# Kernel optimization log

Measured on AMD Instinct MI355X. Metric: run time of the kernel, lower is better.

The kernel has to match this reference:

```python
import jax, jax.numpy as jnp
import numpy as np

BETA = 0.25
TAU = 1.0
NORM_EPS = 1e-06
GUMBEL_EPS = 1e-10


def setup_inputs() -> dict:
    key = jax.random.key(0)
    k1, k2, k3 = jax.random.split(key, 3)
    B, T, D, K = 16, 2048, 512, 2048
    h = jax.random.normal(k1, (B, T, D), dtype=jnp.float32)
    codebook = jax.random.normal(k2, (K, D), dtype=jnp.float32)
    u = jax.random.uniform(k3, (B * T, K), dtype=jnp.float32)  # base uniform for gumbel noise
    return {"h": h, "codebook": codebook, "u": u}


def _l2_normalize(x, eps=NORM_EPS):
    # matches F.normalize(p=2): x / max(||x||, eps)
    n = jnp.linalg.norm(x, axis=-1, keepdims=True)
    return x / jnp.maximum(n, eps)


def reference(h, codebook, u):
    B, T, D = h.shape
    hf = _l2_normalize(h.reshape(-1, D))          # [N, D]
    cb = _l2_normalize(codebook)                  # [K, D]
    # normalized vectors -> squared L2 distance = 2 - 2*cos_sim
    sim = jnp.matmul(hf, cb.T)                    # [N, K]
    distances = 2.0 - 2.0 * sim
    # gumbel_softmax(-distances, tau, hard=False)
    g = -jnp.log(-jnp.log(u + GUMBEL_EPS) + GUMBEL_EPS)
    q = jax.nn.softmax((-distances + g) / TAU, axis=1)  # [N, K]
    indices = jnp.argmax(q, axis=1)               # [N]
    c_tilde = jnp.matmul(q, cb)                   # [N, D] soft code
    c_hard = cb[indices]                          # [N, D] hard code
    codebook_loss = jnp.mean((c_tilde - jax.lax.stop_gradient(hf)) ** 2)
    commitment_loss = jnp.mean((hf - jax.lax.stop_gradient(c_tilde)) ** 2)
    loss = codebook_loss + BETA * commitment_loss
    # straight-through: forward value = c_hard, grads flow through c_tilde and the gather
    c_quantized = c_tilde + c_hard - jax.lax.stop_gradient(c_tilde)
    return (
        q.reshape(B, T, -1),
        c_tilde.reshape(B, T, D),
        c_hard.reshape(B, T, D),
        c_quantized.reshape(B, T, D),
        loss,
        indices.reshape(B, T),
    )
```

## Files before the change

kernel.cpp:

```cpp
#include <hip/hip_runtime.h>
#include <math.h>

#define NROWS 32768
#define DDIM  512
#define KDIM  2048

typedef unsigned short u16;
typedef unsigned int   u32;
using f32x4  = __attribute__((ext_vector_type(4))) float;
using bf16x8 = __attribute__((ext_vector_type(8))) __bf16;

__device__ __forceinline__ u32 rne2(float x, float y) {
    u32 vx = __float_as_uint(x), vy = __float_as_uint(y);
    vx = vx + 0x7fffu + ((vx >> 16) & 1u);
    vy = vy + 0x7fffu + ((vy >> 16) & 1u);
    return (vx >> 16) | (vy & 0xffff0000u);
}

__device__ __forceinline__ void split2(float x, float y, u32 &hp, u32 &lp) {
    u32 ux = __float_as_uint(x), uy = __float_as_uint(y);
    u32 hxm = ux & 0xffff0000u, hym = uy & 0xffff0000u;
    hp = (ux >> 16) | hym;
    float rx = x - __uint_as_float(hxm);
    float ry = y - __uint_as_float(hym);
    lp = rne2(rx, ry);
}

__device__ __forceinline__ float gumbel(float u) {
    return -logf(-logf(u + 1e-10f) + 1e-10f);
}

__global__ __launch_bounds__(256) void rownorms(
    const float* __restrict__ X, float* __restrict__ OUT)
{
    int wv = threadIdx.x >> 6, lane = threadIdx.x & 63;
    int row = blockIdx.x * 4 + wv;
    const float4* src = (const float4*)(X + (size_t)row * DDIM);
    float4 a = src[lane], b = src[lane + 64];
    float ss = a.x*a.x + a.y*a.y + a.z*a.z + a.w*a.w
             + b.x*b.x + b.y*b.y + b.z*b.z + b.w*b.w;
    #pragma unroll
    for (int off = 32; off > 0; off >>= 1) ss += __shfl_down(ss, off, 64);
    if (lane == 0) OUT[row] = 1.0f / fmaxf(sqrtf(ss), 1e-6f);
}

__global__ __launch_bounds__(256) void prep_cb(
    const float* __restrict__ CB, u16* __restrict__ HI, u16* __restrict__ LO,
    float* __restrict__ INVC)
{
    int wv = threadIdx.x >> 6, lane = threadIdx.x & 63;
    int row = blockIdx.x * 4 + wv;
    const float4* src = (const float4*)(CB + (size_t)row * DDIM);
    float4 a = src[lane], b = src[lane + 64];
    float ss = a.x*a.x + a.y*a.y + a.z*a.z + a.w*a.w
             + b.x*b.x + b.y*b.y + b.z*b.z + b.w*b.w;
    #pragma unroll
    for (int off = 32; off > 0; off >>= 1) ss += __shfl_down(ss, off, 64);
    if (lane == 0) INVC[row] = 1.0f / fmaxf(sqrtf(ss), 1e-6f);

    u32 h0, h1, l0, l1;
    split2(a.x, a.y, h0, l0); split2(a.z, a.w, h1, l1);
    *(uint2*)(HI + (size_t)row * DDIM + lane * 4) = make_uint2(h0, h1);
    *(uint2*)(LO + (size_t)row * DDIM + lane * 4) = make_uint2(l0, l1);
    split2(b.x, b.y, h0, l0); split2(b.z, b.w, h1, l1);
    *(uint2*)(HI + (size_t)row * DDIM + 256 + lane * 4) = make_uint2(h0, h1);
    *(uint2*)(LO + (size_t)row * DDIM + 256 + lane * 4) = make_uint2(l0, l1);
}

__global__ __launch_bounds__(256) void transpose_cb(
    const float* __restrict__ CB, const float* __restrict__ INVC,
    u16* __restrict__ CBT)
{
    __shared__ __align__(16) u16 T[64][72];
    int t = threadIdx.x;
    int k0 = blockIdx.x * 64, d0 = blockIdx.y * 64;
    int r = t >> 2, q = (t & 3) * 16;
    float ic = INVC[k0 + r];
    const float* src = CB + (size_t)(k0 + r) * DDIM + d0 + q;
    float4 f0 = *(const float4*)(src);
    float4 f1 = *(const float4*)(src + 4);
    float4 f2 = *(const float4*)(src + 8);
    float4 f3 = *(const float4*)(src + 12);
    f0.x *= ic; f0.y *= ic; f0.z *= ic; f0.w *= ic;
    f1.x *= ic; f1.y *= ic; f1.z *= ic; f1.w *= ic;
    f2.x *= ic; f2.y *= ic; f2.z *= ic; f2.w *= ic;
    f3.x *= ic; f3.y *= ic; f3.z *= ic; f3.w *= ic;
    uint4 p0 = make_uint4(rne2(f0.x,f0.y), rne2(f0.z,f0.w), rne2(f1.x,f1.y), rne2(f1.z,f1.w));
    uint4 p1 = make_uint4(rne2(f2.x,f2.y), rne2(f2.z,f2.w), rne2(f3.x,f3.y), rne2(f3.z,f3.w));
    *(uint4*)&T[r][q]     = p0;
    *(uint4*)&T[r][q + 8] = p1;
    __syncthreads();
    int d = t >> 2, kq = (t & 3) * 16;
    u16 v[16];
    #pragma unroll
    for (int i = 0; i < 16; ++i) v[i] = T[kq + i][d];
    uint4 o0 = make_uint4((u32)v[0]  | ((u32)v[1]  << 16), (u32)v[2]  | ((u32)v[3]  << 16),
                          (u32)v[4]  | ((u32)v[5]  << 16), (u32)v[6]  | ((u32)v[7]  << 16));
    uint4 o1 = make_uint4((u32)v[8]  | ((u32)v[9]  << 16), (u32)v[10] | ((u32)v[11] << 16),
                          (u32)v[12] | ((u32)v[13] << 16), (u32)v[14] | ((u32)v[15] << 16));
    u16* dst = CBT + (size_t)(d0 + d) * KDIM + k0 + kq;
    *(uint4*)dst       = o0;
    *(uint4*)(dst + 8) = o1;
}

#define LDS1 40
__global__ __launch_bounds__(256) void gemm1_split(
    const float* __restrict__ H, const u16* __restrict__ BH,
    const u16* __restrict__ BL, const float* __restrict__ INVH,
    const float* __restrict__ INVC, const float* __restrict__ U,
    float* __restrict__ L)
{
    __shared__ __align__(16) u16 Ah[128 * LDS1];
    __shared__ __align__(16) u16 Al[128 * LDS1];
    __shared__ __align__(16) u16 Bh[128 * LDS1];
    __shared__ __align__(16) u16 Bl[128 * LDS1];

    int t = threadIdx.x;
    int bid = blockIdx.x;
    int w = ((bid & 7) << 9) | (bid >> 3);
    int m0 = (w >> 4) * 128;
    int n0 = (w & 15) * 128;

    int srow = t >> 1;
    int scol = (t & 1) << 4;

    const float* ga  = H  + (size_t)(m0 + srow) * DDIM + scol;
    const u16*   gbh = BH + (size_t)(n0 + srow) * DDIM + scol;
    const u16*   gbl = BL + (size_t)(n0 + srow) * DDIM + scol;

    float4 a0 = *(const float4*)(ga);
    float4 a1 = *(const float4*)(ga + 4);
    float4 a2 = *(const float4*)(ga + 8);
    float4 a3 = *(const float4*)(ga + 12);
    uint4  b0 = *(const uint4*)(gbh);
    uint4  b1 = *(const uint4*)(gbh + 8);
    uint4  c0 = *(const uint4*)(gbl);
    uint4  c1 = *(const uint4*)(gbl + 8);

    f32x4 acc[4][4];
    #pragma unroll
    for (int i = 0; i < 4; ++i)
        #pragma unroll
        for (int j = 0; j < 4; ++j)
            acc[i][j] = (f32x4){0.0f, 0.0f, 0.0f, 0.0f};

    int lane = t & 63;
    int wid  = t >> 6;
    int wr = (wid >> 1) << 6;
    int wc = (wid & 1) << 6;
    int frow = lane & 15;
    int fk   = (lane >> 4) << 3;
    int asb  = srow * LDS1 + scol;

    #pragma unroll 1
    for (int kt = 0; kt < 16; ++kt) {
        uint4 hA, lA;
        split2(a0.x, a0.y, hA.x, lA.x);
        split2(a0.z, a0.w, hA.y, lA.y);
        split2(a1.x, a1.y, hA.z, lA.z);
        split2(a1.z, a1.w, hA.w, lA.w);
        *(uint4*)&Ah[asb] = hA;
        *(uint4*)&Al[asb] = lA;
        split2(a2.x, a2.y, hA.x, lA.x);
        split2(a2.z, a2.w, hA.y, lA.y);
        split2(a3.x, a3.y, hA.z, lA.z);
        split2(a3.z, a3.w, hA.w, lA.w);
        *(uint4*)&Ah[asb + 8] = hA;
        *(uint4*)&Al[asb + 8] = lA;
        *(uint4*)&Bh[asb]     = b0;
        *(uint4*)&Bh[asb + 8] = b1;
        *(uint4*)&Bl[asb]     = c0;
        *(uint4*)&Bl[asb + 8] = c1;
        __syncthreads();
        if (kt < 15) {
            ga += 32; gbh += 32; gbl += 32;
            a0 = *(const float4*)(ga);
            a1 = *(const float4*)(ga + 4);
            a2 = *(const float4*)(ga + 8);
            a3 = *(const float4*)(ga + 12);
            b0 = *(const uint4*)(gbh);
            b1 = *(const uint4*)(gbh + 8);
            c0 = *(const uint4*)(gbl);
            c1 = *(const uint4*)(gbl + 8);
        }
        bf16x8 vbh[4], vbl[4];
        #pragma unroll
        for (int j = 0; j < 4; ++j) {
            int off = (wc + j * 16 + frow) * LDS1 + fk;
            vbh[j] = *(const bf16x8*)&Bh[off];
            vbl[j] = *(const bf16x8*)&Bl[off];
        }
        #pragma unroll
        for (int i = 0; i < 4; ++i) {
            int off = (wr + i * 16 + frow) * LDS1 + fk;
            bf16x8 vah = *(const bf16x8*)&Ah[off];
            bf16x8 val = *(const bf16x8*)&Al[off];
            #pragma unroll
            for (int j = 0; j < 4; ++j) {
                acc[i][j] = __builtin_amdgcn_mfma_f32_16x16x32_bf16(vah, vbh[j], acc[i][j], 0, 0, 0);
                acc[i][j] = __builtin_amdgcn_mfma_f32_16x16x32_bf16(vah, vbl[j], acc[i][j], 0, 0, 0);
                acc[i][j] = __builtin_amdgcn_mfma_f32_16x16x32_bf16(val, vbh[j], acc[i][j], 0, 0, 0);
            }
        }
        __syncthreads();
    }

    float invc[4];
    #pragma unroll
    for (int j = 0; j < 4; ++j) invc[j] = INVC[n0 + wc + j * 16 + frow];
    int r0 = (lane >> 4) << 2;
    #pragma unroll
    for (int i = 0; i < 4; ++i) {
        #pragma unroll
        for (int r = 0; r < 4; ++r) {
            int grow = m0 + wr + i * 16 + r0 + r;
            float ih = INVH[grow];
            const float* urow = U + (size_t)grow * KDIM + n0 + wc + frow;
            float*       lrow = L + (size_t)grow * KDIM + n0 + wc + frow;
            #pragma unroll
            for (int j = 0; j < 4; ++j) {
                float s = acc[i][j][r] * ih * invc[j];
                lrow[j * 16] = 2.0f * s - 2.0f + gumbel(urow[j * 16]);
            }
        }
    }
}

__global__ __launch_bounds__(256) void softmax_rows(
    float* __restrict__ L, float* __restrict__ out_idx_f, int* __restrict__ ws_idx)
{
    int row = blockIdx.x, t = threadIdx.x;
    int lane = t & 63, wv = t >> 6;
    float* lr = L + (size_t)row * KDIM;
    float4 v0 = ((float4*)lr)[t];
    float4 v1 = ((float4*)lr)[t + 256];
    int c0 = t * 4, c1 = 1024 + t * 4;
    float m = v0.x; int mi = c0;
    if (v0.y > m) { m = v0.y; mi = c0 + 1; }
    if (v0.z > m) { m = v0.z; mi = c0 + 2; }
    if (v0.w > m) { m = v0.w; mi = c0 + 3; }
    if (v1.x > m) { m = v1.x; mi = c1; }
    if (v1.y > m) { m = v1.y; mi = c1 + 1; }
    if (v1.z > m) { m = v1.z; mi = c1 + 2; }
    if (v1.w > m) { m = v1.w; mi = c1 + 3; }
    #pragma unroll
    for (int off = 32; off > 0; off >>= 1) {
        float om = __shfl_down(m, off, 64);
        int   oi = __shfl_down(mi, off, 64);
        if (om > m || (om == m && oi < mi)) { m = om; mi = oi; }
    }
    __shared__ float wm[4]; __shared__ int wi[4]; __shared__ float wsum[4];
    if (lane == 0) { wm[wv] = m; wi[wv] = mi; }
    __syncthreads();
    float M = wm[0]; int MI = wi[0];
    #pragma unroll
    for (int k = 1; k < 4; ++k)
        if (wm[k] > M || (wm[k] == M && wi[k] < MI)) { M = wm[k]; MI = wi[k]; }
    v0.x = expf(v0.x - M); v0.y = expf(v0.y - M);
    v0.z = expf(v0.z - M); v0.w = expf(v0.w - M);
    v1.x = expf(v1.x - M); v1.y = expf(v1.y - M);
    v1.z = expf(v1.z - M); v1.w = expf(v1.w - M);
    float s = v0.x + v0.y + v0.z + v0.w + v1.x + v1.y + v1.z + v1.w;
    #pragma unroll
    for (int off = 32; off > 0; off >>= 1) s += __shfl_down(s, off, 64);
    if (lane == 0) wsum[wv] = s;
    __syncthreads();
    float inv = 1.0f / (wsum[0] + wsum[1] + wsum[2] + wsum[3]);
    v0.x *= inv; v0.y *= inv; v0.z *= inv; v0.w *= inv;
    v1.x *= inv; v1.y *= inv; v1.z *= inv; v1.w *= inv;
    ((float4*)lr)[t] = v0;
    ((float4*)lr)[t + 256] = v1;
    if (t == 0) { out_idx_f[row] = (float)MI; ws_idx[row] = MI; }
}

#define LDS2 72
__global__ __launch_bounds__(256) void gemm2_bf16(
    const float* __restrict__ Q, const u16* __restrict__ CBT, float* __restrict__ CT)
{
    __shared__ __align__(16) u16 As[128 * LDS2];
    __shared__ __align__(16) u16 Bs[128 * LDS2];
    int t = threadIdx.x;
    int bid = blockIdx.x;
    int w = ((bid & 7) << 7) | (bid >> 3);
    int m0 = (w >> 2) * 128;
    int n0 = (w & 3) * 128;
    int srow = t >> 1;
    int scol = (t & 1) << 5;
    const float* gq = Q   + (size_t)(m0 + srow) * KDIM + scol;
    const u16*   gb = CBT + (size_t)(n0 + srow) * KDIM + scol;

    float4 q0 = *(const float4*)(gq);
    float4 q1 = *(const float4*)(gq + 4);
    float4 q2 = *(const float4*)(gq + 8);
    float4 q3 = *(const float4*)(gq + 12);
    float4 q4 = *(const float4*)(gq + 16);
    float4 q5 = *(const float4*)(gq + 20);
    float4 q6 = *(const float4*)(gq + 24);
    float4 q7 = *(const float4*)(gq + 28);
    uint4 b0 = *(const uint4*)(gb);
    uint4 b1 = *(const uint4*)(gb + 8);
    uint4 b2 = *(const uint4*)(gb + 16);
    uint4 b3 = *(const uint4*)(gb + 24);

    f32x4 acc[4][4];
    #pragma unroll
    for (int i = 0; i < 4; ++i)
        #pragma unroll
        for (int j = 0; j < 4; ++j)
            acc[i][j] = (f32x4){0.0f, 0.0f, 0.0f, 0.0f};

    int lane = t & 63, wid = t >> 6;
    int wr = (wid >> 1) << 6;
    int wc = (wid & 1) << 6;
    int frow = lane & 15;
    int fk   = (lane >> 4) << 3;
    int asb  = srow * LDS2 + scol;

    #pragma unroll 1
    for (int kt = 0; kt < 32; ++kt) {
        uint4 pa;
        pa = make_uint4(rne2(q0.x,q0.y), rne2(q0.z,q0.w), rne2(q1.x,q1.y), rne2(q1.z,q1.w));
        *(uint4*)&As[asb] = pa;
        pa = make_uint4(rne2(q2.x,q2.y), rne2(q2.z,q2.w), rne2(q3.x,q3.y), rne2(q3.z,q3.w));
        *(uint4*)&As[asb + 8] = pa;
        pa = make_uint4(rne2(q4.x,q4.y), rne2(q4.z,q4.w), rne2(q5.x,q5.y), rne2(q5.z,q5.w));
        *(uint4*)&As[asb + 16] = pa;
        pa = make_uint4(rne2(q6.x,q6.y), rne2(q6.z,q6.w), rne2(q7.x,q7.y), rne2(q7.z,q7.w));
        *(uint4*)&As[asb + 24] = pa;
        *(uint4*)&Bs[asb]      = b0;
        *(uint4*)&Bs[asb + 8]  = b1;
        *(uint4*)&Bs[asb + 16] = b2;
        *(uint4*)&Bs[asb + 24] = b3;
        __syncthreads();
        if (kt < 31) {
            gq += 64; gb += 64;
            q0 = *(const float4*)(gq);
            q1 = *(const float4*)(gq + 4);
            q2 = *(const float4*)(gq + 8);
            q3 = *(const float4*)(gq + 12);
            q4 = *(const float4*)(gq + 16);
            q5 = *(const float4*)(gq + 20);
            q6 = *(const float4*)(gq + 24);
            q7 = *(const float4*)(gq + 28);
            b0 = *(const uint4*)(gb);
            b1 = *(const uint4*)(gb + 8);
            b2 = *(const uint4*)(gb + 16);
            b3 = *(const uint4*)(gb + 24);
        }
        #pragma unroll
        for (int kk = 0; kk < 2; ++kk) {
            bf16x8 vb[4];
            #pragma unroll
            for (int j = 0; j < 4; ++j)
                vb[j] = *(const bf16x8*)&Bs[(wc + j * 16 + frow) * LDS2 + kk * 32 + fk];
            #pragma unroll
            for (int i = 0; i < 4; ++i) {
                bf16x8 va = *(const bf16x8*)&As[(wr + i * 16 + frow) * LDS2 + kk * 32 + fk];
                #pragma unroll
                for (int j = 0; j < 4; ++j)
                    acc[i][j] = __builtin_amdgcn_mfma_f32_16x16x32_bf16(va, vb[j], acc[i][j], 0, 0, 0);
            }
        }
        __syncthreads();
    }

    int r0 = (lane >> 4) << 2;
    #pragma unroll
    for (int i = 0; i < 4; ++i) {
        #pragma unroll
        for (int r = 0; r < 4; ++r) {
            int grow = m0 + wr + i * 16 + r0 + r;
            float* crow = CT + (size_t)grow * DDIM + n0 + wc + frow;
            #pragma unroll
            for (int j = 0; j < 4; ++j) crow[j * 16] = acc[i][j][r];
        }
    }
}

__global__ __launch_bounds__(256) void gather_loss(
    const u16* __restrict__ CBH, const u16* __restrict__ CBL,
    const float* __restrict__ INVC, const int* __restrict__ ws_idx,
    const float* __restrict__ Ct, const float* __restrict__ H,
    const float* __restrict__ INVH,
    float* __restrict__ c_hard, float* __restrict__ c_quant,
    float* __restrict__ partials)
{
    int row = blockIdx.x, t = threadIdx.x;
    int idx = ws_idx[row];
    float ic = INVC[idx], ih = INVH[row];
    u32 hp = ((const u32*)(CBH + (size_t)idx * DDIM))[t];
    u32 lp = ((const u32*)(CBL + (size_t)idx * DDIM))[t];
    float cx = (__uint_as_float(hp << 16) + __uint_as_float(lp << 16)) * ic;
    float cy = (__uint_as_float(hp & 0xffff0000u) + __uint_as_float(lp & 0xffff0000u)) * ic;
    float2 cv; cv.x = cx; cv.y = cy;
    ((float2*)(c_hard  + (size_t)row * DDIM))[t] = cv;
    ((float2*)(c_quant + (size_t)row * DDIM))[t] = cv;
    float2 hv = ((const float2*)(H  + (size_t)row * DDIM))[t];
    float2 ct = ((const float2*)(Ct + (size_t)row * DDIM))[t];
    float dx = ct.x - hv.x * ih, dy = ct.y - hv.y * ih;
    __shared__ float red[256];
    red[t] = dx * dx + dy * dy;
    __syncthreads();
    for (int s = 128; s > 0; s >>= 1) {
        if (t < s) red[t] += red[t + s];
        __syncthreads();
    }
    if (t == 0) partials[row] = red[0];
}

__global__ __launch_bounds__(1024) void loss_reduce(
    const float* __restrict__ partials, float* __restrict__ loss_out)
{
    int t = threadIdx.x;
    float s = 0.0f;
    for (int i = t; i < NROWS; i += 1024) s += partials[i];
    __shared__ float red[1024];
    red[t] = s;
    __syncthreads();
    for (int st = 512; st > 0; st >>= 1) {
        if (t < st) red[t] += red[t + st];
        __syncthreads();
    }
    if (t == 0) loss_out[0] = red[0] * (1.25f / ((float)NROWS * (float)DDIM));
}

extern "C" void kernel_launch(void* const* d_in, const int* in_sizes, int n_in,
                              void* d_out, int out_size, void* d_ws, size_t ws_size,
                              hipStream_t stream) {
    const float* h  = (const float*)d_in[0];
    const float* cb = (const float*)d_in[1];
    const float* u  = (const float*)d_in[2];

    float* out     = (float*)d_out;
    float* q       = out;
    float* c_tilde = out + (size_t)NROWS * KDIM;
    float* c_hard  = c_tilde + (size_t)NROWS * DDIM;
    float* c_quant = c_hard  + (size_t)NROWS * DDIM;
    float* loss    = c_quant + (size_t)NROWS * DDIM;
    float* idx_f   = loss + 1;

    u16* cb_hi = (u16*)d_ws;
    u16* cb_lo = cb_hi + (size_t)KDIM * DDIM;
    u16* cbT   = cb_lo + (size_t)KDIM * DDIM;
    float* invn_h  = (float*)(cbT + (size_t)KDIM * DDIM);
    float* invn_cb = invn_h + NROWS;
    int*   ws_idx  = (int*)(invn_cb + KDIM);
    float* partials = (float*)(ws_idx + NROWS);

    rownorms<<<NROWS / 4, 256, 0, stream>>>(h, invn_h);
    prep_cb<<<KDIM / 4, 256, 0, stream>>>(cb, cb_hi, cb_lo, invn_cb);
    transpose_cb<<<dim3(KDIM / 64, DDIM / 64), 256, 0, stream>>>(cb, invn_cb, cbT);

    gemm1_split<<<(NROWS / 128) * (KDIM / 128), 256, 0, stream>>>(
        h, cb_hi, cb_lo, invn_h, invn_cb, u, q);

    softmax_rows<<<NROWS, 256, 0, stream>>>(q, idx_f, ws_idx);

    gemm2_bf16<<<(NROWS / 128) * (DDIM / 128), 256, 0, stream>>>(q, cbT, c_tilde);

    gather_loss<<<NROWS, 256, 0, stream>>>(cb_hi, cb_lo, invn_cb, ws_idx,
                                           c_tilde, h, invn_h,
                                           c_hard, c_quant, partials);
    loss_reduce<<<1, 1024, 0, stream>>>(partials, loss);
}
```

Measured before the change: 1.182 ms.

## Pre-split h to bf16 hi/lo and use direct-to-LDS loads in both GEMMs

The row-norm kernel now also writes bf16 hi/lo halves of h, so the first GEMM can stream pre-split bf16 tiles with global_load_lds into a double-buffered, XOR-swizzled LDS layout instead of converting fp32 on the fly. The softmax optionally writes unnormalized bf16 exponentials plus a per-row inverse sum, and a new second GEMM reads those half-width values and scales at the end, avoiding re-reading fp32 q. Each path is chosen by workspace size, with the old kernels kept as fallbacks. The cost is extra workspace traffic to write the split h and the exponential buffer, plus slightly different rounding in c_tilde.

```diff
diff --git a/kernel.cpp b/kernel.cpp
--- a/kernel.cpp
+++ b/kernel.cpp
@@ -30,8 +30,16 @@
     return -logf(-logf(u + 1e-10f) + 1e-10f);
 }
 
-__global__ __launch_bounds__(256) void rownorms(
-    const float* __restrict__ X, float* __restrict__ OUT)
+__device__ __forceinline__ void gload16(const void* g, void* l) {
+    __builtin_amdgcn_global_load_lds(
+        (const __attribute__((address_space(1))) void*)g,
+        (__attribute__((address_space(3))) void*)l,
+        16, 0, 0);
+}
+
+__global__ __launch_bounds__(256) void rownorms_h(
+    const float* __restrict__ X, float* __restrict__ OUT,
+    u16* __restrict__ HI, u16* __restrict__ LO, int do_split)
 {
     int wv = threadIdx.x >> 6, lane = threadIdx.x & 63;
     int row = blockIdx.x * 4 + wv;
@@ -42,6 +50,15 @@
     #pragma unroll
     for (int off = 32; off > 0; off >>= 1) ss += __shfl_down(ss, off, 64);
     if (lane == 0) OUT[row] = 1.0f / fmaxf(sqrtf(ss), 1e-6f);
+    if (do_split) {
+        u32 h0, h1, l0, l1;
+        split2(a.x, a.y, h0, l0); split2(a.z, a.w, h1, l1);
+        *(uint2*)(HI + (size_t)row * DDIM + lane * 4) = make_uint2(h0, h1);
+        *(uint2*)(LO + (size_t)row * DDIM + lane * 4) = make_uint2(l0, l1);
+        split2(b.x, b.y, h0, l0); split2(b.z, b.w, h1, l1);
+        *(uint2*)(HI + (size_t)row * DDIM + 256 + lane * 4) = make_uint2(h0, h1);
+        *(uint2*)(LO + (size_t)row * DDIM + 256 + lane * 4) = make_uint2(l0, l1);
+    }
 }
 
 __global__ __launch_bounds__(256) void prep_cb(
@@ -101,6 +118,111 @@
     u16* dst = CBT + (size_t)(d0 + d) * KDIM + k0 + kq;
     *(uint4*)dst       = o0;
     *(uint4*)(dst + 8) = o1;
+}
+
+__global__ __launch_bounds__(256) void gemm1_mfma(
+    const u16* __restrict__ AH, const u16* __restrict__ AL,
+    const u16* __restrict__ BHc, const u16* __restrict__ BLc,
+    const float* __restrict__ INVH, const float* __restrict__ INVC,
+    const float* __restrict__ U, float* __restrict__ L)
+{
+    __shared__ __align__(16) u16 S1[2][4][4096];
+    int t = threadIdx.x;
+    int lane = t & 63, w = t >> 6;
+    int bid = blockIdx.x;
+    int wg = ((bid & 7) << 9) | (bid >> 3);
+    int m0 = (wg >> 4) << 7;
+    int n0 = (wg & 15) << 7;
+
+    int sl0 = (t & 7) ^ ((t >> 3) & 7);
+    int r0 = ((t >> 3) << 1) + (sl0 >> 2), c0 = sl0 & 3;
+    int s1i = t + 256;
+    int sl1 = (s1i & 7) ^ ((s1i >> 3) & 7);
+    int r1 = ((s1i >> 3) << 1) + (sl1 >> 2), c1 = sl1 & 3;
+
+    const u16* gA0h = AH  + (size_t)(m0 + r0) * DDIM + c0 * 8;
+    const u16* gA1h = AH  + (size_t)(m0 + r1) * DDIM + c1 * 8;
+    const u16* gA0l = AL  + (size_t)(m0 + r0) * DDIM + c0 * 8;
+    const u16* gA1l = AL  + (size_t)(m0 + r1) * DDIM + c1 * 8;
+    const u16* gB0h = BHc + (size_t)(n0 + r0) * DDIM + c0 * 8;
+    const u16* gB1h = BHc + (size_t)(n0 + r1) * DDIM + c1 * 8;
+    const u16* gB0l = BLc + (size_t)(n0 + r0) * DDIM + c0 * 8;
+    const u16* gB1l = BLc + (size_t)(n0 + r1) * DDIM + c1 * 8;
+
+    int d0 = w * 512, d1 = w * 512 + 2048;
+
+    int wr = (w >> 1) << 6, wc = (w & 1) << 6;
+    int frow = lane & 15, ck = lane >> 4;
+    int offA[4], offB[4];
+    #pragma unroll
+    for (int i = 0; i < 4; ++i) {
+        int R  = wr + i * 16 + frow;
+        offA[i] = (R >> 1) * 64 + (((((R & 1) << 2) | ck) ^ ((R >> 1) & 7)) << 3);
+        int Rb = wc + i * 16 + frow;
+        offB[i] = (Rb >> 1) * 64 + (((((Rb & 1) << 2) | ck) ^ ((Rb >> 1) & 7)) << 3);
+    }
+
+    f32x4 acc[4][4];
+    #pragma unroll
+    for (int i = 0; i < 4; ++i)
+        #pragma unroll
+        for (int j = 0; j < 4; ++j)
+            acc[i][j] = (f32x4){0.0f, 0.0f, 0.0f, 0.0f};
+
+#define STAGE1(bs, ko) do { \
+    gload16(gA0h + (ko), &S1[bs][0][d0]); gload16(gA1h + (ko), &S1[bs][0][d1]); \
+    gload16(gA0l + (ko), &S1[bs][1][d0]); gload16(gA1l + (ko), &S1[bs][1][d1]); \
+    gload16(gB0h + (ko), &S1[bs][2][d0]); gload16(gB1h + (ko), &S1[bs][2][d1]); \
+    gload16(gB0l + (ko), &S1[bs][3][d0]); gload16(gB1l + (ko), &S1[bs][3][d1]); \
+} while (0)
+
+    STAGE1(0, 0);
+    __syncthreads();
+    int cur = 0;
+    #pragma unroll 1
+    for (int kt = 0; kt < 16; ++kt) {
+        if (kt < 15) STAGE1(cur ^ 1, (kt + 1) * 32);
+        bf16x8 vbh[4], vbl[4];
+        #pragma unroll
+        for (int j = 0; j < 4; ++j) {
+            vbh[j] = *(const bf16x8*)&S1[cur][2][offB[j]];
+            vbl[j] = *(const bf16x8*)&S1[cur][3][offB[j]];
+        }
+        #pragma unroll
+        for (int i = 0; i < 4; ++i) {
+            bf16x8 vah = *(const bf16x8*)&S1[cur][0][offA[i]];
+            bf16x8 val = *(const bf16x8*)&S1[cur][1][offA[i]];
+            #pragma unroll
+            for (int j = 0; j < 4; ++j) {
+                acc[i][j] = __builtin_amdgcn_mfma_f32_16x16x32_bf16(vah, vbh[j], acc[i][j], 0, 0, 0);
+                acc[i][j] = __builtin_amdgcn_mfma_f32_16x16x32_bf16(vah, vbl[j], acc[i][j], 0, 0, 0);
+                acc[i][j] = __builtin_amdgcn_mfma_f32_16x16x32_bf16(val, vbh[j], acc[i][j], 0, 0, 0);
+            }
+        }
+        __syncthreads();
+        cur ^= 1;
+    }
+#undef STAGE1
+
+    float invc[4];
+    #pragma unroll
+    for (int j = 0; j < 4; ++j) invc[j] = INVC[n0 + wc + j * 16 + frow];
+    int rr0 = ck << 2;
+    #pragma unroll
+    for (int i = 0; i < 4; ++i) {
+        #pragma unroll
+        for (int r = 0; r < 4; ++r) {
+            int grow = m0 + wr + i * 16 + rr0 + r;
+            float ih = INVH[grow];
+            const float* urow = U + (size_t)grow * KDIM + n0 + wc + frow;
+            float*       lrow = L + (size_t)grow * KDIM + n0 + wc + frow;
+            #pragma unroll
+            for (int j = 0; j < 4; ++j) {
+                float s = acc[i][j][r] * ih * invc[j];
+                lrow[j * 16] = 2.0f * s - 2.0f + gumbel(urow[j * 16]);
+            }
+        }
+    }
 }
 
 #define LDS1 40
@@ -227,7 +349,8 @@
 }
 
 __global__ __launch_bounds__(256) void softmax_rows(
-    float* __restrict__ L, float* __restrict__ out_idx_f, int* __restrict__ ws_idx)
+    float* __restrict__ L, float* __restrict__ out_idx_f, int* __restrict__ ws_idx,
+    u16* __restrict__ E, float* __restrict__ SINV, int we)
 {
     int row = blockIdx.x, t = threadIdx.x;
     int lane = t & 63, wv = t >> 6;
@@ -266,11 +389,116 @@
     if (lane == 0) wsum[wv] = s;
     __syncthreads();
     float inv = 1.0f / (wsum[0] + wsum[1] + wsum[2] + wsum[3]);
+    if (we) {
+        *(uint2*)(E + (size_t)row * KDIM + 4 * t) =
+            make_uint2(rne2(v0.x, v0.y), rne2(v0.z, v0.w));
+        *(uint2*)(E + (size_t)row * KDIM + 1024 + 4 * t) =
+            make_uint2(rne2(v1.x, v1.y), rne2(v1.z, v1.w));
+        if (t == 0) SINV[row] = inv;
+    }
     v0.x *= inv; v0.y *= inv; v0.z *= inv; v0.w *= inv;
     v1.x *= inv; v1.y *= inv; v1.z *= inv; v1.w *= inv;
     ((float4*)lr)[t] = v0;
     ((float4*)lr)[t + 256] = v1;
     if (t == 0) { out_idx_f[row] = (float)MI; ws_idx[row] = MI; }
+}
+
+__global__ __launch_bounds__(256) void gemm2_e(
+    const u16* __restrict__ E, const u16* __restrict__ CBT,
+    const float* __restrict__ SINV, float* __restrict__ CT)
+{
+    __shared__ __align__(16) u16 S2[2][2][8192];
+    int t = threadIdx.x;
+    int lane = t & 63, w = t >> 6;
+    int bid = blockIdx.x;
+    int wg = ((bid & 7) << 7) | (bid >> 3);
+    int m0 = (wg >> 2) << 7;
+    int n0 = (wg & 3) << 7;
+
+    int rr[4], cc[4];
+    #pragma unroll
+    for (int I = 0; I < 4; ++I) {
+        int s = t + I * 256;
+        rr[I] = s >> 3;
+        cc[I] = (s & 7) ^ (rr[I] & 7);
+    }
+    const u16* ge0 = E   + (size_t)(m0 + rr[0]) * KDIM + cc[0] * 8;
+    const u16* ge1 = E   + (size_t)(m0 + rr[1]) * KDIM + cc[1] * 8;
+    const u16* ge2 = E   + (size_t)(m0 + rr[2]) * KDIM + cc[2] * 8;
+    const u16* ge3 = E   + (size_t)(m0 + rr[3]) * KDIM + cc[3] * 8;
+    const u16* gb0 = CBT + (size_t)(n0 + rr[0]) * KDIM + cc[0] * 8;
+    const u16* gb1 = CBT + (size_t)(n0 + rr[1]) * KDIM + cc[1] * 8;
+    const u16* gb2 = CBT + (size_t)(n0 + rr[2]) * KDIM + cc[2] * 8;
+    const u16* gb3 = CBT + (size_t)(n0 + rr[3]) * KDIM + cc[3] * 8;
+
+    int dA0 = w * 512, dA1 = w * 512 + 2048, dA2 = w * 512 + 4096, dA3 = w * 512 + 6144;
+
+    int wr = (w >> 1) << 6, wc = (w & 1) << 6;
+    int frow = lane & 15, ck = lane >> 4;
+    int offA[4][2], offB[4][2];
+    #pragma unroll
+    for (int i = 0; i < 4; ++i) {
+        int R  = wr + i * 16 + frow;
+        int Rb = wc + i * 16 + frow;
+        #pragma unroll
+        for (int kk = 0; kk < 2; ++kk) {
+            int ch = kk * 4 + ck;
+            offA[i][kk] = R  * 64 + ((ch ^ (R  & 7)) << 3);
+            offB[i][kk] = Rb * 64 + ((ch ^ (Rb & 7)) << 3);
+        }
+    }
+
+    f32x4 acc[4][4];
+    #pragma unroll
+    for (int i = 0; i < 4; ++i)
+        #pragma unroll
+        for (int j = 0; j < 4; ++j)
+            acc[i][j] = (f32x4){0.0f, 0.0f, 0.0f, 0.0f};
+
+#define STAGE2(bs, ko) do { \
+    gload16(ge0 + (ko), &S2[bs][0][dA0]); gload16(ge1 + (ko), &S2[bs][0][dA1]); \
+    gload16(ge2 + (ko), &S2[bs][0][dA2]); gload16(ge3 + (ko), &S2[bs][0][dA3]); \
+    gload16(gb0 + (ko), &S2[bs][1][dA0]); gload16(gb1 + (ko), &S2[bs][1][dA1]); \
+    gload16(gb2 + (ko), &S2[bs][1][dA2]); gload16(gb3 + (ko), &S2[bs][1][dA3]); \
+} while (0)
+
+    STAGE2(0, 0);
+    __syncthreads();
+    int cur = 0;
+    #pragma unroll 1
+    for (int kt = 0; kt < 32; ++kt) {
+        if (kt < 31) STAGE2(cur ^ 1, (kt + 1) * 64);
+        #pragma unroll
+        for (int kk = 0; kk < 2; ++kk) {
+            bf16x8 vb[4];
+            #pragma unroll
+            for (int j = 0; j < 4; ++j)
+                vb[j] = *(const bf16x8*)&S2[cur][1][offB[j][kk]];
+            #pragma unroll
+            for (int i = 0; i < 4; ++i) {
+                bf16x8 va = *(const bf16x8*)&S2[cur][0][offA[i][kk]];
+                #pragma unroll
+                for (int j = 0; j < 4; ++j)
+                    acc[i][j] = __builtin_amdgcn_mfma_f32_16x16x32_bf16(va, vb[j], acc[i][j], 0, 0, 0);
+            }
+        }
+        __syncthreads();
+        cur ^= 1;
+    }
+#undef STAGE2
+
+    int rr0 = ck << 2;
+    #pragma unroll
+    for (int i = 0; i < 4; ++i) {
+        #pragma unroll
+        for (int r = 0; r < 4; ++r) {
+            int grow = m0 + wr + i * 16 + rr0 + r;
+            float sv = SINV[grow];
+            float* crow = CT + (size_t)grow * DDIM + n0 + wc + frow;
+            #pragma unroll
+            for (int j = 0; j < 4; ++j) crow[j * 16] = acc[i][j][r] * sv;
+        }
+    }
 }
 
 #define LDS2 72
@@ -439,24 +667,40 @@
     float* loss    = c_quant + (size_t)NROWS * DDIM;
     float* idx_f   = loss + 1;
 
-    u16* cb_hi = (u16*)d_ws;
-    u16* cb_lo = cb_hi + (size_t)KDIM * DDIM;
-    u16* cbT   = cb_lo + (size_t)KDIM * DDIM;
-    float* invn_h  = (float*)(cbT + (size_t)KDIM * DDIM);
-    float* invn_cb = invn_h + NROWS;
-    int*   ws_idx  = (int*)(invn_cb + KDIM);
-    float* partials = (float*)(ws_idx + NROWS);
-
-    rownorms<<<NROWS / 4, 256, 0, stream>>>(h, invn_h);
+    char* wsp = (char*)d_ws;
+    u16* cb_hi = (u16*)wsp;            wsp += (size_t)KDIM * DDIM * 2;
+    u16* cb_lo = (u16*)wsp;            wsp += (size_t)KDIM * DDIM * 2;
+    u16* cbT   = (u16*)wsp;            wsp += (size_t)DDIM * KDIM * 2;
+    float* invn_h  = (float*)wsp;      wsp += (size_t)NROWS * 4;
+    float* invn_cb = (float*)wsp;      wsp += (size_t)KDIM * 4;
+    float* sinv    = (float*)wsp;      wsp += (size_t)NROWS * 4;
+    int*   ws_idx  = (int*)wsp;        wsp += (size_t)NROWS * 4;
+    float* partials= (float*)wsp;      wsp += (size_t)NROWS * 4;
+    u16* h_hi = (u16*)wsp;             wsp += (size_t)NROWS * DDIM * 2;
+    u16* h_lo = (u16*)wsp;             wsp += (size_t)NROWS * DDIM * 2;
+    u16* Ebuf = (u16*)wsp;
+
+    const size_t NEED_B = 73932800ull;
+    const size_t NEED_A = 208150528ull;
+    int tier = (ws_size >= NEED_A) ? 0 : ((ws_size >= NEED_B) ? 1 : 2);
+
+    rownorms_h<<<NROWS / 4, 256, 0, stream>>>(h, invn_h, h_hi, h_lo, tier <= 1);
     prep_cb<<<KDIM / 4, 256, 0, stream>>>(cb, cb_hi, cb_lo, invn_cb);
     transpose_cb<<<dim3(KDIM / 64, DDIM / 64), 256, 0, stream>>>(cb, invn_cb, cbT);
 
-    gemm1_split<<<(NROWS / 128) * (KDIM / 128), 256, 0, stream>>>(
-        h, cb_hi, cb_lo, invn_h, invn_cb, u, q);
-
-    softmax_rows<<<NROWS, 256, 0, stream>>>(q, idx_f, ws_idx);
-
-    gemm2_bf16<<<(NROWS / 128) * (DDIM / 128), 256, 0, stream>>>(q, cbT, c_tilde);
+    if (tier <= 1)
+        gemm1_mfma<<<(NROWS / 128) * (KDIM / 128), 256, 0, stream>>>(
+            h_hi, h_lo, cb_hi, cb_lo, invn_h, invn_cb, u, q);
+    else
+        gemm1_split<<<(NROWS / 128) * (KDIM / 128), 256, 0, stream>>>(
+            h, cb_hi, cb_lo, invn_h, invn_cb, u, q);
+
+    softmax_rows<<<NROWS, 256, 0, stream>>>(q, idx_f, ws_idx, Ebuf, sinv, tier == 0);
+
+    if (tier == 0)
+        gemm2_e<<<(NROWS / 128) * (DDIM / 128), 256, 0, stream>>>(Ebuf, cbT, sinv, c_tilde);
+    else
+        gemm2_bf16<<<(NROWS / 128) * (DDIM / 128), 256, 0, stream>>>(q, cbT, c_tilde);
 
     gather_loss<<<NROWS, 256, 0, stream>>>(cb_hi, cb_lo, invn_cb, ws_idx,
                                            c_tilde, h, invn_h,
```

After: 1.115 ms. 5.7% less time.
